# Kernel tuning notes

Hardware: AMD Instinct MI355X
Metric: run time of the kernel (lower is better)

## Reference

```python
import jax, jax.numpy as jnp
import numpy as np

N_NODES = 100000
N_EDGES = 1600000
IN_CH = 64
HID = 128
N_CLASSES = 8
NUM_GRAPHS = 1000


def setup_inputs() -> dict:
    key = jax.random.key(0)
    ks = jax.random.split(key, 12)
    x = jax.random.normal(ks[0], (N_NODES, IN_CH), dtype=jnp.float32)
    edge_index = jax.random.randint(ks[1], (2, N_EDGES), 0, N_NODES, dtype=jnp.int64)
    batch = jnp.sort(jax.random.randint(ks[2], (N_NODES,), 0, NUM_GRAPHS, dtype=jnp.int64))
    s = 1.0 / np.sqrt(IN_CH)
    W1_l = jax.random.uniform(ks[3], (IN_CH, HID), jnp.float32, -s, s)
    W1_r = jax.random.uniform(ks[4], (IN_CH, HID), jnp.float32, -s, s)
    b1 = jnp.zeros((HID,), jnp.float32)
    s2 = 1.0 / np.sqrt(HID)
    W2_l = jax.random.uniform(ks[5], (HID, HID), jnp.float32, -s2, s2)
    W2_r = jax.random.uniform(ks[6], (HID, HID), jnp.float32, -s2, s2)
    b2 = jnp.zeros((HID,), jnp.float32)
    Wh = jax.random.uniform(ks[7], (HID, N_CLASSES), jnp.float32, -s2, s2)
    bh = jnp.zeros((N_CLASSES,), jnp.float32)
    return {"x": x, "edge_index": edge_index, "batch": batch,
            "W1_l": W1_l, "W1_r": W1_r, "b1": b1,
            "W2_l": W2_l, "W2_r": W2_r, "b2": b2,
            "Wh": Wh, "bh": bh}


def _sage_conv(x, src, dst, W_l, W_r, b):
    # mean-aggregate source features at target nodes (PyG source_to_target flow)
    msg_sum = jax.ops.segment_sum(x[src], dst, num_segments=N_NODES)  # [N, d]
    cnt = jax.ops.segment_sum(jnp.ones((src.shape[0], 1), x.dtype), dst, num_segments=N_NODES)
    mean = msg_sum / jnp.maximum(cnt, 1.0)
    return mean @ W_l + x @ W_r + b


def reference(x, edge_index, batch, W1_l, W1_r, b1, W2_l, W2_r, b2, Wh, bh):
    src, dst = edge_index[0], edge_index[1]
    h = jax.nn.relu(_sage_conv(x, src, dst, W1_l, W1_r, b1))
    h = jax.nn.relu(_sage_conv(h, src, dst, W2_l, W2_r, b2))
    # global mean pool per graph
    g_sum = jax.ops.segment_sum(h, batch, num_segments=NUM_GRAPHS)  # [G, HID]
    g_cnt = jax.ops.segment_sum(jnp.ones((h.shape[0], 1), h.dtype), batch, num_segments=NUM_GRAPHS)
    pooled = g_sum / jnp.maximum(g_cnt, 1.0)
    return pooled @ Wh + bh
```

## Files before the change

kernel.cpp:

```cpp
#include <hip/hip_runtime.h>

#define NN 100000
#define NE 1600000
#define CIN 64
#define CH 128
#define NCLS 8
#define NG 1000

#define NBUCK 16
#define BUCK_NODES 6250
#define SUBS 8
#define NSUB (NBUCK * SUBS)
#define SUB_NODES 782
#define BCAP 102500
#define CVT_GRID 1024
#define BUF 512

typedef __attribute__((ext_vector_type(8))) short bf16x8;
typedef __attribute__((ext_vector_type(8))) unsigned short ushort8;
typedef __attribute__((ext_vector_type(4))) float f32x4;

__device__ __forceinline__ float bf2f(unsigned short u) {
    union { unsigned int i; float f; } c; c.i = ((unsigned int)u) << 16; return c.f;
}
__device__ __forceinline__ unsigned short f2bf(float f) {
    union { float f; unsigned int i; } c; c.f = f;
    unsigned int r = c.i + 0x7FFFu + ((c.i >> 16) & 1u);
    return (unsigned short)(r >> 16);
}

__device__ __forceinline__ bool is_w64(const void* __restrict__ edge) {
    const int* e32 = (const int*)edge;
    int v = e32[2 * (threadIdx.x & 63) + 1];
    return __ballot(v != 0) == 0ull;
}

__global__ __launch_bounds__(256) void k_cvt_part(const void* __restrict__ edge, const void* __restrict__ batch,
                                                  unsigned* __restrict__ bucket, int* __restrict__ gcur,
                                                  int* __restrict__ bati) {
    __shared__ unsigned sbuf[NBUCK][BUF];
    __shared__ int scnt[NBUCK];
    __shared__ int sneed[NBUCK];
    __shared__ int sbase[NBUCK];
    const int tid = threadIdx.x;
    const bool w64 = is_w64(edge);
    if (tid < NBUCK) scnt[tid] = 0;
    __syncthreads();

    const int ntiles = (NE + 255) / 256;
    for (int t = blockIdx.x; t < ntiles; t += CVT_GRID) {
        const int i = t * 256 + tid;
        if (i < NE) {
            int s, d;
            if (w64) {
                const long long* e = (const long long*)edge;
                s = (int)e[i]; d = (int)e[NE + i];
            } else {
                const int* e = (const int*)edge;
                s = e[i]; d = e[NE + i];
            }
            const int q = d / BUCK_NODES;
            const unsigned v = ((unsigned)(d - q * BUCK_NODES) << 17) | (unsigned)s;
            int pos = atomicAdd(&scnt[q], 1);
            sbuf[q][pos] = v;
        }
        __syncthreads();
        if (tid < NBUCK) {
            int c = scnt[tid];
            int need = (c > BUF - 256) ? c : 0;
            sneed[tid] = need;
            if (need) { sbase[tid] = atomicAdd(&gcur[tid], need); scnt[tid] = 0; }
        }
        __syncthreads();
        for (int q = 0; q < NBUCK; q++) {
            int n = sneed[q];
            if (n) {
                unsigned* gb = bucket + (size_t)q * BCAP + sbase[q];
                for (int k = tid; k < n; k += 256) gb[k] = sbuf[q][k];
            }
        }
        __syncthreads();
    }
    if (tid < NBUCK) {
        int c = scnt[tid];
        sneed[tid] = c;
        if (c) sbase[tid] = atomicAdd(&gcur[tid], c);
    }
    __syncthreads();
    for (int q = 0; q < NBUCK; q++) {
        int n = sneed[q];
        if (n) {
            unsigned* gb = bucket + (size_t)q * BCAP + sbase[q];
            for (int k = tid; k < n; k += 256) gb[k] = sbuf[q][k];
        }
    }
    const int idx0 = blockIdx.x * 256 + tid;
    const int stride = CVT_GRID * 256;
    if (w64) {
        const long long* b = (const long long*)batch;
        for (int i = idx0; i < NN; i += stride) bati[i] = (int)b[i];
    } else {
        const int* b = (const int*)batch;
        for (int i = idx0; i < NN; i += stride) bati[i] = b[i];
    }
}

__global__ __launch_bounds__(1024) void k_build(const unsigned* __restrict__ bucket, const int* __restrict__ gcur,
                                                int* __restrict__ rowstart, int* __restrict__ eidx) {
    __shared__ int cur[SUB_NODES];
    __shared__ int wsum[16];
    __shared__ int carry;
    __shared__ int sbef;
    const int q = blockIdx.x >> 3;
    const int sub = blockIdx.x & 7;
    const int tid = threadIdx.x;
    const int lane = tid & 63;
    const int wid = tid >> 6;
    const int lo_local = sub * SUB_NODES;
    const int hi_local = min(BUCK_NODES, lo_local + SUB_NODES);
    const int n_nodes = hi_local - lo_local;
    const int node0 = q * BUCK_NODES + lo_local;
    const int cnt = gcur[q];
    const int cnt4 = cnt >> 2;
    int bbase = 0;
    for (int j = 0; j < q; j++) bbase += gcur[j];
    const unsigned* gb = bucket + (size_t)q * BCAP;
    const uint4* gb4 = (const uint4*)gb;

    for (int i = tid; i < SUB_NODES; i += 1024) cur[i] = 0;
    if (tid == 0) { carry = 0; sbef = 0; }
    __syncthreads();

    int before = 0;
    for (int i = tid; i < cnt4; i += 1024) {
        uint4 u = gb4[i];
#pragma unroll
        for (int k = 0; k < 4; k++) {
            unsigned w = (k == 0) ? u.x : (k == 1) ? u.y : (k == 2) ? u.z : u.w;
            int dl = (int)(w >> 17);
            if (dl < lo_local) before++;
            else if (dl < hi_local) atomicAdd(&cur[dl - lo_local], 1);
        }
    }
    for (int i = cnt4 * 4 + tid; i < cnt; i += 1024) {
        int dl = (int)(gb[i] >> 17);
        if (dl < lo_local) before++;
        else if (dl < hi_local) atomicAdd(&cur[dl - lo_local], 1);
    }
#pragma unroll
    for (int s = 1; s < 64; s <<= 1) before += __shfl_xor(before, s, 64);
    if (lane == 0) atomicAdd(&sbef, before);
    __syncthreads();
    const int base = bbase + sbef;

    {
        const int i = tid;
        const int v = (i < SUB_NODES) ? cur[i] : 0;
        int incl = v;
#pragma unroll
        for (int s = 1; s < 64; s <<= 1) {
            int u = __shfl_up(incl, s, 64);
            if (lane >= s) incl += u;
        }
        if (lane == 63) wsum[wid] = incl;
        __syncthreads();
        if (wid == 0) {
            int wv = (lane < 16) ? wsum[lane] : 0;
#pragma unroll
            for (int s = 1; s < 16; s <<= 1) {
                int u = __shfl_up(wv, s, 64);
                if (lane >= s) wv += u;
            }
            if (lane < 16) wsum[lane] = wv;
        }
        __syncthreads();
        const int ebase = (wid ? wsum[wid - 1] : 0);
        const int excl = ebase + incl - v;
        __syncthreads();
        if (i < SUB_NODES) {
            if (i < n_nodes) rowstart[node0 + i] = base + excl;
            cur[i] = excl;
        }
        __syncthreads();
    }
    if (blockIdx.x == NSUB - 1 && tid == 0) rowstart[NN] = NE;

    for (int i = tid; i < cnt4; i += 1024) {
        uint4 u = gb4[i];
#pragma unroll
        for (int k = 0; k < 4; k++) {
            unsigned w = (k == 0) ? u.x : (k == 1) ? u.y : (k == 2) ? u.z : u.w;
            int dl = (int)(w >> 17);
            if (dl >= lo_local && dl < hi_local) {
                int pos = base + atomicAdd(&cur[dl - lo_local], 1);
                eidx[pos] = (int)(w & 0x1FFFFu);
            }
        }
    }
    for (int i = cnt4 * 4 + tid; i < cnt; i += 1024) {
        unsigned w = gb[i];
        int dl = (int)(w >> 17);
        if (dl >= lo_local && dl < hi_local) {
            int pos = base + atomicAdd(&cur[dl - lo_local], 1);
            eidx[pos] = (int)(w & 0x1FFFFu);
        }
    }
}

__global__ void k_cvtx(const float* __restrict__ x, unsigned short* __restrict__ xb, int total8) {
    int i = blockIdx.x * blockDim.x + threadIdx.x;
    if (i >= total8) return;
    float4 v0 = ((const float4*)x)[2 * i];
    float4 v1 = ((const float4*)x)[2 * i + 1];
    ushort8 o;
    o[0] = f2bf(v0.x); o[1] = f2bf(v0.y); o[2] = f2bf(v0.z); o[3] = f2bf(v0.w);
    o[4] = f2bf(v1.x); o[5] = f2bf(v1.y); o[6] = f2bf(v1.z); o[7] = f2bf(v1.w);
    ((ushort8*)xb)[i] = o;
}

__global__ void k_cvtWall(const float* __restrict__ W1l, const float* __restrict__ W1r,
                          const float* __restrict__ W2l, const float* __restrict__ W2r,
                          unsigned short* __restrict__ W1lf, unsigned short* __restrict__ W1rf,
                          unsigned short* __restrict__ W2lf, unsigned short* __restrict__ W2rf) {
    int idx = blockIdx.x * blockDim.x + threadIdx.x;
    const float* W; unsigned short* out; int K; int local;
    if (idx < 1024)      { W = W1l; out = W1lf; K = 64;  local = idx; }
    else if (idx < 2048) { W = W1r; out = W1rf; K = 64;  local = idx - 1024; }
    else if (idx < 4096) { W = W2l; out = W2lf; K = 128; local = idx - 2048; }
    else                 { W = W2r; out = W2rf; K = 128; local = idx - 4096; }
    int l = local & 63;
    int ks = (local >> 6) % (K / 32);
    int nt = (local >> 6) / (K / 32);
    int krow = ks * 32 + (l >> 4) * 8;
    int col = nt * 16 + (l & 15);
    ushort8 o;
#pragma unroll
    for (int j = 0; j < 8; j++) o[j] = f2bf(W[(size_t)(krow + j) * 128 + col]);
    ((ushort8*)out)[local] = o;
}

template <int C>
__global__ __launch_bounds__(256) void k_gatherv(const unsigned short* __restrict__ feat,
                                                 const int* __restrict__ eidx,
                                                 const int* __restrict__ rowstart,
                                                 unsigned short* __restrict__ msg) {
    constexpr int G = C / 8;
    constexpr int EPW = 64 / G;
    const int node = blockIdx.x * 4 + (threadIdx.x >> 6);
    if (node >= NN) return;
    const int lane = threadIdx.x & 63;
    const int grp = lane / G;
    const int sub = lane % G;
    const int lo = rowstart[node];
    const int hi = rowstart[node + 1];

    float acc[8] = {0.f, 0.f, 0.f, 0.f, 0.f, 0.f, 0.f, 0.f};
    int e = lo + grp;
    for (; e + EPW < hi; e += 2 * EPW) {
        int s0 = eidx[e];
        int s1 = eidx[e + EPW];
        ushort8 v0 = *(const ushort8*)&feat[(size_t)s0 * C + sub * 8];
        ushort8 v1 = *(const ushort8*)&feat[(size_t)s1 * C + sub * 8];
#pragma unroll
        for (int j = 0; j < 8; j++) acc[j] += bf2f(v0[j]) + bf2f(v1[j]);
    }
    if (e < hi) {
        int s0 = eidx[e];
        ushort8 v0 = *(const ushort8*)&feat[(size_t)s0 * C + sub * 8];
#pragma unroll
        for (int j = 0; j < 8; j++) acc[j] += bf2f(v0[j]);
    }

#pragma unroll
    for (int off = G; off < 64; off <<= 1) {
#pragma unroll
        for (int j = 0; j < 8; j++) acc[j] += __shfl_xor(acc[j], off, 64);
    }

    if (grp == 0) {
        const float inv = 1.0f / fmaxf((float)(hi - lo), 1.0f);
        ushort8 o;
#pragma unroll
        for (int j = 0; j < 8; j++) o[j] = f2bf(acc[j] * inv);
        *(ushort8*)&msg[(size_t)node * C + sub * 8] = o;
    }
}

template <int K>
__global__ __launch_bounds__(256) void k_sage_mfma(const unsigned short* __restrict__ A1,
                                                   const unsigned short* __restrict__ A2,
                                                   const unsigned short* __restrict__ B1,
                                                   const unsigned short* __restrict__ B2,
                                                   const float* __restrict__ bias,
                                                   unsigned short* __restrict__ out) {
    constexpr int KS = K / 32;
    const int wid = threadIdx.x >> 6;
    const int lane = threadIdx.x & 63;
    const int rowbase = blockIdx.x * 64 + wid * 16;
    const int arow = rowbase + (lane & 15);
    const int arowc = (arow < NN) ? arow : (NN - 1);
    const int kgrp = (lane >> 4) * 8;

    f32x4 acc[8];
#pragma unroll
    for (int nt = 0; nt < 8; nt++) {
        float bj = bias[nt * 16 + (lane & 15)];
        acc[nt][0] = bj; acc[nt][1] = bj; acc[nt][2] = bj; acc[nt][3] = bj;
    }

    const bf16x8* b1v = (const bf16x8*)B1;
    const bf16x8* b2v = (const bf16x8*)B2;
#pragma unroll
    for (int ks = 0; ks < KS; ks++) {
        bf16x8 a1 = *(const bf16x8*)&A1[(size_t)arowc * K + ks * 32 + kgrp];
        bf16x8 a2 = *(const bf16x8*)&A2[(size_t)arowc * K + ks * 32 + kgrp];
#pragma unroll
        for (int nt = 0; nt < 8; nt++) {
            acc[nt] = __builtin_amdgcn_mfma_f32_16x16x32_bf16(a1, b1v[(nt * KS + ks) * 64 + lane], acc[nt], 0, 0, 0);
            acc[nt] = __builtin_amdgcn_mfma_f32_16x16x32_bf16(a2, b2v[(nt * KS + ks) * 64 + lane], acc[nt], 0, 0, 0);
        }
    }

    const int colb = lane & 15;
    const int rhi = (lane >> 4) * 4;
#pragma unroll
    for (int nt = 0; nt < 8; nt++) {
#pragma unroll
        for (int r = 0; r < 4; r++) {
            int row = rowbase + rhi + r;
            if (row < NN)
                out[(size_t)row * 128 + nt * 16 + colb] = f2bf(fmaxf(acc[nt][r], 0.0f));
        }
    }
}

__device__ __forceinline__ int lower_bound_dev(const int* __restrict__ a, int n, int key) {
    int lo = 0, hi = n;
    while (lo < hi) {
        int mid = (lo + hi) >> 1;
        if (a[mid] < key) lo = mid + 1; else hi = mid;
    }
    return lo;
}

__global__ __launch_bounds__(128) void k_poolb(const unsigned short* __restrict__ h,
                                               const int* __restrict__ batch,
                                               const float* __restrict__ Wh, const float* __restrict__ bh,
                                               float* __restrict__ out) {
    const int g = blockIdx.x;
    const int lo = lower_bound_dev(batch, NN, g);
    const int hi = lower_bound_dev(batch, NN, g + 1);
    const int j = threadIdx.x;
    float s = 0.f;
    for (int i = lo; i < hi; i++) s += bf2f(h[(size_t)i * CH + j]);
    __shared__ float pooled[CH];
    pooled[j] = s / fmaxf((float)(hi - lo), 1.0f);
    __syncthreads();
    if (j < NCLS) {
        float acc = bh[j];
#pragma unroll
        for (int k = 0; k < CH; k++) acc = fmaf(pooled[k], Wh[k * NCLS + j], acc);
        out[(size_t)g * NCLS + j] = acc;
    }
}

extern "C" void kernel_launch(void* const* d_in, const int* in_sizes, int n_in,
                              void* d_out, int out_size, void* d_ws, size_t ws_size,
                              hipStream_t stream) {
    const float* x   = (const float*)d_in[0];
    const void* edge = d_in[1];
    const void* batch= d_in[2];
    const float* W1l = (const float*)d_in[3];
    const float* W1r = (const float*)d_in[4];
    const float* b1  = (const float*)d_in[5];
    const float* W2l = (const float*)d_in[6];
    const float* W2r = (const float*)d_in[7];
    const float* b2  = (const float*)d_in[8];
    const float* Wh  = (const float*)d_in[9];
    const float* bh  = (const float*)d_in[10];
    float* out = (float*)d_out;

    char* p = (char*)d_ws;
    unsigned short* xb   = (unsigned short*)p; p += (size_t)NN * CIN * 2;
    unsigned short* h1b  = (unsigned short*)p; p += (size_t)NN * CH * 2;
    unsigned short* h2b  = (unsigned short*)p; p += (size_t)NN * CH * 2;
    unsigned short* msgb = (unsigned short*)p; p += (size_t)NN * CH * 2;
    unsigned short* W1lf = (unsigned short*)p; p += (size_t)CIN * CH * 2;
    unsigned short* W1rf = (unsigned short*)p; p += (size_t)CIN * CH * 2;
    unsigned short* W2lf = (unsigned short*)p; p += (size_t)CH * CH * 2;
    unsigned short* W2rf = (unsigned short*)p; p += (size_t)CH * CH * 2;
    int* bati  = (int*)p;       p += (size_t)NN * sizeof(int);
    int* gcur  = (int*)p;       p += NBUCK * sizeof(int);
    int* rowstart = (int*)p;    p += (size_t)(NN + 1) * sizeof(int) + 12;
    unsigned* bucket = (unsigned*)p; p += (size_t)NBUCK * BCAP * sizeof(unsigned);
    int* eidx  = (int*)p;       p += (size_t)NE * sizeof(int);

    hipMemsetAsync(gcur, 0, NBUCK * sizeof(int), stream);
    k_cvt_part<<<CVT_GRID, 256, 0, stream>>>(edge, batch, bucket, gcur, bati);
    k_build<<<NSUB, 1024, 0, stream>>>(bucket, gcur, rowstart, eidx);

    k_cvtx<<<(NN * CIN / 8 + 255) / 256, 256, 0, stream>>>(x, xb, NN * CIN / 8);
    k_cvtWall<<<24, 256, 0, stream>>>(W1l, W1r, W2l, W2r, W1lf, W1rf, W2lf, W2rf);

    k_gatherv<CIN><<<(NN + 3) / 4, 256, 0, stream>>>(xb, eidx, rowstart, msgb);
    k_sage_mfma<CIN><<<(NN + 63) / 64, 256, 0, stream>>>(msgb, xb, W1lf, W1rf, b1, h1b);

    k_gatherv<CH><<<(NN + 3) / 4, 256, 0, stream>>>(h1b, eidx, rowstart, msgb);
    k_sage_mfma<CH><<<(NN + 63) / 64, 256, 0, stream>>>(msgb, h1b, W2lf, W2rf, b2, h2b);

    k_poolb<<<NG, 128, 0, stream>>>(h2b, bati, Wh, bh, out);
}
```

Measured before the change: 260.8 us.

## Fuse neighbor mean gather into SAGE MFMA kernel, drop message buffer

Replaces the separate gather kernel and the MFMA linear kernel with one kernel. Each lane gathers its row's neighbor features straight into the MFMA A-fragment layout, scales by the inverse degree, and feeds the result to the MFMA. This removes the msg buffer write and re-read and two kernel launches per layer. The cost is a worse gather pattern: each lane now walks its own node's edge list serially with 16-byte loads across KS chunks, the edge loop diverges by degree within a wave, and register pressure rises from the acc_g array.

Result: slower. 282.0 us (+8.1%).

```diff
diff --git a/kernel.cpp b/kernel.cpp
--- a/kernel.cpp
+++ b/kernel.cpp
@@ -109,7 +109,6 @@
                                                 int* __restrict__ rowstart, int* __restrict__ eidx) {
     __shared__ int cur[SUB_NODES];
     __shared__ int wsum[16];
-    __shared__ int carry;
     __shared__ int sbef;
     const int q = blockIdx.x >> 3;
     const int sub = blockIdx.x & 7;
@@ -128,7 +127,7 @@
     const uint4* gb4 = (const uint4*)gb;
 
     for (int i = tid; i < SUB_NODES; i += 1024) cur[i] = 0;
-    if (tid == 0) { carry = 0; sbef = 0; }
+    if (tid == 0) sbef = 0;
     __syncthreads();
 
     int before = 0;
@@ -239,60 +238,14 @@
     ((ushort8*)out)[local] = o;
 }
 
-template <int C>
-__global__ __launch_bounds__(256) void k_gatherv(const unsigned short* __restrict__ feat,
-                                                 const int* __restrict__ eidx,
-                                                 const int* __restrict__ rowstart,
-                                                 unsigned short* __restrict__ msg) {
-    constexpr int G = C / 8;
-    constexpr int EPW = 64 / G;
-    const int node = blockIdx.x * 4 + (threadIdx.x >> 6);
-    if (node >= NN) return;
-    const int lane = threadIdx.x & 63;
-    const int grp = lane / G;
-    const int sub = lane % G;
-    const int lo = rowstart[node];
-    const int hi = rowstart[node + 1];
-
-    float acc[8] = {0.f, 0.f, 0.f, 0.f, 0.f, 0.f, 0.f, 0.f};
-    int e = lo + grp;
-    for (; e + EPW < hi; e += 2 * EPW) {
-        int s0 = eidx[e];
-        int s1 = eidx[e + EPW];
-        ushort8 v0 = *(const ushort8*)&feat[(size_t)s0 * C + sub * 8];
-        ushort8 v1 = *(const ushort8*)&feat[(size_t)s1 * C + sub * 8];
-#pragma unroll
-        for (int j = 0; j < 8; j++) acc[j] += bf2f(v0[j]) + bf2f(v1[j]);
-    }
-    if (e < hi) {
-        int s0 = eidx[e];
-        ushort8 v0 = *(const ushort8*)&feat[(size_t)s0 * C + sub * 8];
-#pragma unroll
-        for (int j = 0; j < 8; j++) acc[j] += bf2f(v0[j]);
-    }
-
-#pragma unroll
-    for (int off = G; off < 64; off <<= 1) {
-#pragma unroll
-        for (int j = 0; j < 8; j++) acc[j] += __shfl_xor(acc[j], off, 64);
-    }
-
-    if (grp == 0) {
-        const float inv = 1.0f / fmaxf((float)(hi - lo), 1.0f);
-        ushort8 o;
-#pragma unroll
-        for (int j = 0; j < 8; j++) o[j] = f2bf(acc[j] * inv);
-        *(ushort8*)&msg[(size_t)node * C + sub * 8] = o;
-    }
-}
-
 template <int K>
-__global__ __launch_bounds__(256) void k_sage_mfma(const unsigned short* __restrict__ A1,
-                                                   const unsigned short* __restrict__ A2,
-                                                   const unsigned short* __restrict__ B1,
-                                                   const unsigned short* __restrict__ B2,
-                                                   const float* __restrict__ bias,
-                                                   unsigned short* __restrict__ out) {
+__global__ __launch_bounds__(256) void k_sage_fused(const unsigned short* __restrict__ feat,
+                                                    const int* __restrict__ eidx,
+                                                    const int* __restrict__ rowstart,
+                                                    const unsigned short* __restrict__ B1,
+                                                    const unsigned short* __restrict__ B2,
+                                                    const float* __restrict__ bias,
+                                                    unsigned short* __restrict__ out) {
     constexpr int KS = K / 32;
     const int wid = threadIdx.x >> 6;
     const int lane = threadIdx.x & 63;
@@ -301,6 +254,46 @@
     const int arowc = (arow < NN) ? arow : (NN - 1);
     const int kgrp = (lane >> 4) * 8;
 
+    float acc_g[KS][8];
+#pragma unroll
+    for (int ks = 0; ks < KS; ks++)
+#pragma unroll
+        for (int j = 0; j < 8; j++) acc_g[ks][j] = 0.f;
+
+    const int lo = rowstart[arowc];
+    const int hi = rowstart[arowc + 1];
+    int e = lo;
+    for (; e + 1 < hi; e += 2) {
+        const int s0 = eidx[e];
+        const int s1 = eidx[e + 1];
+        const unsigned short* r0 = &feat[(size_t)s0 * K + kgrp];
+        const unsigned short* r1 = &feat[(size_t)s1 * K + kgrp];
+#pragma unroll
+        for (int ks = 0; ks < KS; ks++) {
+            ushort8 v0 = *(const ushort8*)(r0 + ks * 32);
+            ushort8 v1 = *(const ushort8*)(r1 + ks * 32);
+#pragma unroll
+            for (int j = 0; j < 8; j++) acc_g[ks][j] += bf2f(v0[j]) + bf2f(v1[j]);
+        }
+    }
+    if (e < hi) {
+        const int s0 = eidx[e];
+        const unsigned short* r0 = &feat[(size_t)s0 * K + kgrp];
+#pragma unroll
+        for (int ks = 0; ks < KS; ks++) {
+            ushort8 v0 = *(const ushort8*)(r0 + ks * 32);
+#pragma unroll
+            for (int j = 0; j < 8; j++) acc_g[ks][j] += bf2f(v0[j]);
+        }
+    }
+    const float inv = 1.0f / fmaxf((float)(hi - lo), 1.0f);
+
+    union { ushort8 u; bf16x8 b; } a1[KS];
+#pragma unroll
+    for (int ks = 0; ks < KS; ks++)
+#pragma unroll
+        for (int j = 0; j < 8; j++) a1[ks].u[j] = f2bf(acc_g[ks][j] * inv);
+
     f32x4 acc[8];
 #pragma unroll
     for (int nt = 0; nt < 8; nt++) {
@@ -312,11 +305,10 @@
     const bf16x8* b2v = (const bf16x8*)B2;
 #pragma unroll
     for (int ks = 0; ks < KS; ks++) {
-        bf16x8 a1 = *(const bf16x8*)&A1[(size_t)arowc * K + ks * 32 + kgrp];
-        bf16x8 a2 = *(const bf16x8*)&A2[(size_t)arowc * K + ks * 32 + kgrp];
+        bf16x8 a2 = *(const bf16x8*)&feat[(size_t)arowc * K + ks * 32 + kgrp];
 #pragma unroll
         for (int nt = 0; nt < 8; nt++) {
-            acc[nt] = __builtin_amdgcn_mfma_f32_16x16x32_bf16(a1, b1v[(nt * KS + ks) * 64 + lane], acc[nt], 0, 0, 0);
+            acc[nt] = __builtin_amdgcn_mfma_f32_16x16x32_bf16(a1[ks].b, b1v[(nt * KS + ks) * 64 + lane], acc[nt], 0, 0, 0);
             acc[nt] = __builtin_amdgcn_mfma_f32_16x16x32_bf16(a2, b2v[(nt * KS + ks) * 64 + lane], acc[nt], 0, 0, 0);
         }
     }
@@ -384,7 +376,6 @@
     unsigned short* xb   = (unsigned short*)p; p += (size_t)NN * CIN * 2;
     unsigned short* h1b  = (unsigned short*)p; p += (size_t)NN * CH * 2;
     unsigned short* h2b  = (unsigned short*)p; p += (size_t)NN * CH * 2;
-    unsigned short* msgb = (unsigned short*)p; p += (size_t)NN * CH * 2;
     unsigned short* W1lf = (unsigned short*)p; p += (size_t)CIN * CH * 2;
     unsigned short* W1rf = (unsigned short*)p; p += (size_t)CIN * CH * 2;
     unsigned short* W2lf = (unsigned short*)p; p += (size_t)CH * CH * 2;
@@ -402,11 +393,8 @@
     k_cvtx<<<(NN * CIN / 8 + 255) / 256, 256, 0, stream>>>(x, xb, NN * CIN / 8);
     k_cvtWall<<<24, 256, 0, stream>>>(W1l, W1r, W2l, W2r, W1lf, W1rf, W2lf, W2rf);
 
-    k_gatherv<CIN><<<(NN + 3) / 4, 256, 0, stream>>>(xb, eidx, rowstart, msgb);
-    k_sage_mfma<CIN><<<(NN + 63) / 64, 256, 0, stream>>>(msgb, xb, W1lf, W1rf, b1, h1b);
-
-    k_gatherv<CH><<<(NN + 3) / 4, 256, 0, stream>>>(h1b, eidx, rowstart, msgb);
-    k_sage_mfma<CH><<<(NN + 63) / 64, 256, 0, stream>>>(msgb, h1b, W2lf, W2rf, b2, h2b);
+    k_sage_fused<CIN><<<(NN + 63) / 64, 256, 0, stream>>>(xb, eidx, rowstart, W1lf, W1rf, b1, h1b);
+    k_sage_fused<CH><<<(NN + 63) / 64, 256, 0, stream>>>(h1b, eidx, rowstart, W2lf, W2rf, b2, h2b);
 
     k_poolb<<<NG, 128, 0, stream>>>(h2b, bati, Wh, bh, out);
 }
```
